# Kernel tuning notes

Hardware: AMD Instinct MI355X
Metric: run time of the kernel (lower is better)

The kernel has to match this reference:

```python
import jax, jax.numpy as jnp
import numpy as np

D_EMB = 512
N_HEADS = 8
D_K = 64
D_V = 64
D_FF = 2048
N_LAYERS = 6
VOCAB = 32000
SRC_LEN = 512


def sin_enc_table(n_position, d):
    pos = jnp.arange(n_position, dtype=jnp.float32)[:, None]
    j = jnp.arange(d, dtype=jnp.float32)[None, :]
    angle = pos / jnp.power(10000.0, 2.0 * jnp.floor(j / 2.0) / d)
    return jnp.where((jnp.arange(d) % 2 == 0)[None, :], jnp.sin(angle), jnp.cos(angle))


def layer_norm(x, gamma, beta, eps=1e-5):
    mu = jnp.mean(x, axis=-1, keepdims=True)
    var = jnp.mean(jnp.square(x - mu), axis=-1, keepdims=True)
    return (x - mu) * jax.lax.rsqrt(var + eps) * gamma + beta


def setup_inputs() -> dict:
    key = jax.random.key(0)
    ks = jax.random.split(key, 20)
    s = 0.02
    L = N_LAYERS
    inp = {
        'enc_inputs': jax.random.randint(ks[0], (16, 512), 0, VOCAB),
        'emb': jax.random.normal(ks[1], (VOCAB, D_EMB), jnp.float32) * s,
        'Wq': jax.random.normal(ks[2], (L, N_HEADS * D_K, D_EMB), jnp.float32) * s,
        'bq': jnp.zeros((L, N_HEADS * D_K), jnp.float32),
        'Wk': jax.random.normal(ks[3], (L, N_HEADS * D_K, D_EMB), jnp.float32) * s,
        'bk': jnp.zeros((L, N_HEADS * D_K), jnp.float32),
        'Wv': jax.random.normal(ks[4], (L, N_HEADS * D_V, D_EMB), jnp.float32) * s,
        'bv': jnp.zeros((L, N_HEADS * D_V), jnp.float32),
        'Wo': jax.random.normal(ks[5], (L, D_EMB, N_HEADS * D_V), jnp.float32) * s,
        'bo': jnp.zeros((L, D_EMB), jnp.float32),
        'g1': jnp.ones((L, D_EMB), jnp.float32),
        'b1': jnp.zeros((L, D_EMB), jnp.float32),
        'Wc1': jax.random.normal(ks[6], (L, D_FF, D_EMB), jnp.float32) * s,
        'bc1': jnp.zeros((L, D_FF), jnp.float32),
        'Wc2': jax.random.normal(ks[7], (L, D_EMB, D_FF), jnp.float32) * s,
        'bc2': jnp.zeros((L, D_EMB), jnp.float32),
        'g2': jnp.ones((L, D_EMB), jnp.float32),
        'b2': jnp.zeros((L, D_EMB), jnp.float32),
    }
    return inp


def encoder_fwd(enc_inputs, emb, Wq, bq, Wk, bk, Wv, bv, Wo, bo, g1, b1, Wc1, bc1, Wc2, bc2, g2, b2):
    B, S = enc_inputs.shape
    pos_table = sin_enc_table(SRC_LEN + 1, D_EMB)  # frozen
    x = emb[enc_inputs] + pos_table[jnp.arange(1, S + 1)][None, :, :]
    # pad mask: True where key token == 0; broadcast over heads and queries
    pad = (enc_inputs == 0)[:, None, None, :]  # [B,1,1,S]
    scale = 1.0 / np.sqrt(D_K)
    attn_weights = []
    for l in range(N_LAYERS):
        residual = x
        q = (x @ Wq[l].T + bq[l]).reshape(B, S, N_HEADS, D_K).transpose(0, 2, 1, 3)
        k = (x @ Wk[l].T + bk[l]).reshape(B, S, N_HEADS, D_K).transpose(0, 2, 1, 3)
        v = (x @ Wv[l].T + bv[l]).reshape(B, S, N_HEADS, D_V).transpose(0, 2, 1, 3)
        scores = jnp.einsum('bhqd,bhkd->bhqk', q, k) * scale
        scores = jnp.where(pad, -1e9, scores)
        w = jax.nn.softmax(scores, axis=-1)
        ctx = jnp.einsum('bhqk,bhkd->bhqd', w, v)
        ctx = ctx.transpose(0, 2, 1, 3).reshape(B, S, N_HEADS * D_V)
        x = layer_norm(ctx @ Wo[l].T + bo[l] + residual, g1[l], b1[l])
        # position-wise FFN (conv1d k=1 == dense)
        h = jax.nn.relu(x @ Wc1[l].T + bc1[l])
        x = layer_norm(h @ Wc2[l].T + bc2[l] + x, g2[l], b2[l])
        attn_weights.append(w)
    return x, jnp.stack(attn_weights)


def reference(enc_inputs, emb, Wq, bq, Wk, bk, Wv, bv, Wo, bo, g1, b1, Wc1, bc1, Wc2, bc2, g2, b2):
    return encoder_fwd(enc_inputs, emb, Wq, bq, Wk, bk, Wv, bv, Wo, bo, g1, b1, Wc1, bc1, Wc2, bc2, g2, b2)
```

## Files before the change

### kernel.cpp

```cpp
#include <hip/hip_runtime.h>

typedef unsigned short u16;
typedef __attribute__((ext_vector_type(8))) short s16x8;
typedef __attribute__((ext_vector_type(4))) float f32x4;
typedef __attribute__((ext_vector_type(4))) unsigned short u16x4;

#define DEVI __device__ __forceinline__

DEVI float bf2f(u16 h) { union { unsigned u; float f; } v; v.u = ((unsigned)h) << 16; return v.f; }
DEVI u16 f2bf(float f) {
  union { unsigned u; float f; } v; v.f = f;
  unsigned u = v.u;
  unsigned r = (u + 0x7fffu + ((u >> 16) & 1u)) >> 16;
  return (u16)r;
}

DEVI f32x4 mfma16(s16x8 a, s16x8 b, f32x4 c) {
  return __builtin_amdgcn_mfma_f32_16x16x32_bf16(a, b, c, 0, 0, 0);
}

__global__ void cvt_kern(const float* __restrict__ in, u16* __restrict__ out, int n4) {
  for (int i = blockIdx.x * blockDim.x + threadIdx.x; i < n4; i += gridDim.x * blockDim.x) {
    f32x4 v = ((const f32x4*)in)[i];
    u16x4 o = { f2bf(v[0]), f2bf(v[1]), f2bf(v[2]), f2bf(v[3]) };
    ((u16x4*)out)[i] = o;
  }
}

__global__ void cvt_qkv_kern(const float* __restrict__ Wq, const float* __restrict__ Wk,
                             const float* __restrict__ Wv, u16* __restrict__ Wout) {
  int total = 6 * 1536 * 512 / 8;
  for (int idx = blockIdx.x * blockDim.x + threadIdx.x; idx < total; idx += gridDim.x * blockDim.x) {
    int c8 = idx & 63;
    int t = idx >> 6;
    int r = t % 1536, l = t / 1536;
    const float* src; int rr = r;
    if (r < 512) src = Wq;
    else if (r < 1024) { src = Wk; rr = r - 512; }
    else { src = Wv; rr = r - 1024; }
    const f32x4* p = (const f32x4*)(src + ((size_t)(l * 512 + rr) * 512) + c8 * 8);
    f32x4 a = p[0], b = p[1];
    u16x4 o0 = { f2bf(a[0]), f2bf(a[1]), f2bf(a[2]), f2bf(a[3]) };
    u16x4 o1 = { f2bf(b[0]), f2bf(b[1]), f2bf(b[2]), f2bf(b[3]) };
    u16x4* q = (u16x4*)(Wout + (size_t)idx * 8);
    q[0] = o0; q[1] = o1;
  }
}

__global__ void biasqkv_kern(const float* __restrict__ bq, const float* __restrict__ bk,
                             const float* __restrict__ bv, float* __restrict__ bout) {
  int i = blockIdx.x * 256 + threadIdx.x;
  if (i >= 6 * 1536) return;
  int l = i / 1536, r = i % 1536;
  float v = (r < 512) ? bq[l * 512 + r] : (r < 1024) ? bk[l * 512 + r - 512] : bv[l * 512 + r - 1024];
  bout[i] = v;
}

__global__ void embed_kern(const int* __restrict__ tok, const float* __restrict__ emb,
                           float* __restrict__ x, u16* __restrict__ xb) {
  int bs = blockIdx.x;
  int s = bs & 511;
  int t = threadIdx.x;
  int id = tok[bs];
  float pos = (float)(s + 1);
  int j0 = t * 4;
  f32x4 e = *(const f32x4*)(emb + (size_t)id * 512 + j0);
  f32x4 o; u16x4 ob;
  #pragma unroll
  for (int u = 0; u < 4; ++u) {
    int j = j0 + u;
    float expo = (float)(j & ~1) * (1.0f / 512.0f);
    float ang = pos / powf(10000.0f, expo);
    float pe = (j & 1) ? cosf(ang) : sinf(ang);
    float v = e[u] + pe;
    o[u] = v; ob[u] = f2bf(v);
  }
  *(f32x4*)(x + (size_t)bs * 512 + j0) = o;
  *(u16x4*)(xb + (size_t)bs * 512 + j0) = ob;
}

template <int WM, bool RELU, bool F32OUT>
__global__ __launch_bounds__(256, 2) void gemm_bs(const u16* __restrict__ A,
                                                  const u16* __restrict__ Bt,
                                                  const float* __restrict__ bias,
                                                  float* __restrict__ Pf, u16* __restrict__ Cb,
                                                  int N, int K, int nN) {
  constexpr int MF = WM / 16;
  constexpr int RPB = WM * 4;
  __shared__ __align__(16) u16 Bsw[128 * 256];

  const int chunkw = gridDim.x >> 3;
  const int wgid = (blockIdx.x & 7) * chunkw + (blockIdx.x >> 3);
  const int n = wgid % nN, m = wgid / nN;
  const int bn0 = n * 128, bm0 = m * RPB;

  const int tid = threadIdx.x, lane = tid & 63, wid = tid >> 6;
  const int l15 = lane & 15, lhi = lane >> 4;
  const int mrow0 = bm0 + wid * WM;

  f32x4 acc[MF][8];
  #pragma unroll
  for (int i = 0; i < MF; ++i)
    #pragma unroll
    for (int j = 0; j < 8; ++j)
      #pragma unroll
      for (int r = 0; r < 4; ++r) acc[i][j][r] = 0.0f;

  const u16* aB[MF];
  #pragma unroll
  for (int i = 0; i < MF; ++i)
    aB[i] = A + (size_t)(mrow0 + i * 16 + l15) * K + lhi * 8;

  const int rounds = K >> 8;
  for (int r = 0; r < rounds; ++r) {
    const int kb = r << 8;
    s16x8 tmp[16];
    #pragma unroll
    for (int c = 0; c < 16; ++c) {
      int cc = c * 256 + tid;
      int row = cc >> 5, col = cc & 31;
      tmp[c] = *(const s16x8*)(Bt + (size_t)(bn0 + row) * K + kb + col * 8);
    }
    __syncthreads();
    #pragma unroll
    for (int c = 0; c < 16; ++c) {
      int cc = c * 256 + tid;
      int row = cc >> 5, col = cc & 31;
      int byte = row * 512 + ((col * 16) ^ ((row & 7) << 4));
      *(s16x8*)((char*)Bsw + byte) = tmp[c];
    }
    __syncthreads();
    #pragma unroll
    for (int ks = 0; ks < 8; ++ks) {
      s16x8 af[MF], bf[8];
      #pragma unroll
      for (int i = 0; i < MF; ++i)
        af[i] = *(const s16x8*)(aB[i] + kb + ks * 32);
      #pragma unroll
      for (int j = 0; j < 8; ++j) {
        int row = j * 16 + l15;
        int byte = row * 512 + (((ks * 64) + lhi * 16) ^ ((row & 7) << 4));
        bf[j] = *(const s16x8*)((char*)Bsw + byte);
      }
      #pragma unroll
      for (int i = 0; i < MF; ++i)
        #pragma unroll
        for (int j = 0; j < 8; ++j)
          acc[i][j] = mfma16(af[i], bf[j], acc[i][j]);
    }
  }

  const int r0 = mrow0 + lhi * 4;
  const int c0 = bn0 + l15;
  #pragma unroll
  for (int i = 0; i < MF; ++i)
    #pragma unroll
    for (int j = 0; j < 8; ++j) {
      int col = c0 + j * 16;
      float bv = F32OUT ? 0.0f : bias[col];
      #pragma unroll
      for (int r = 0; r < 4; ++r) {
        int row = r0 + i * 16 + r;
        float v = acc[i][j][r] + bv;
        if (RELU) v = fmaxf(v, 0.0f);
        if (F32OUT) Pf[(size_t)row * N + col] = v;
        else Cb[(size_t)row * N + col] = f2bf(v);
      }
    }
}

__global__ void ln2_kern(const float* __restrict__ parts,
                         const float* __restrict__ bias, const float* __restrict__ resid,
                         const float* __restrict__ gam, const float* __restrict__ bet,
                         float* __restrict__ out, u16* __restrict__ outb) {
  int row = blockIdx.x * 4 + (threadIdx.x >> 6);
  int t = threadIdx.x & 63;
  size_t base = (size_t)row * 512;
  const f32x4* p0 = (const f32x4*)(parts + base);
  f32x4 v0 = p0[t], v1 = p0[t + 64];
  const f32x4* bp2 = (const f32x4*)bias;
  f32x4 bia = bp2[t], bib = bp2[t + 64];
  const f32x4* rp = (const f32x4*)(resid + base);
  f32x4 rr0 = rp[t], rr1 = rp[t + 64];
  #pragma unroll
  for (int u = 0; u < 4; ++u) { v0[u] += bia[u] + rr0[u]; v1[u] += bib[u] + rr1[u]; }

  float s = v0[0] + v0[1] + v0[2] + v0[3] + v1[0] + v1[1] + v1[2] + v1[3];
  float q = v0[0]*v0[0] + v0[1]*v0[1] + v0[2]*v0[2] + v0[3]*v0[3]
          + v1[0]*v1[0] + v1[1]*v1[1] + v1[2]*v1[2] + v1[3]*v1[3];
  #pragma unroll
  for (int d = 1; d < 64; d <<= 1) { s += __shfl_xor(s, d, 64); q += __shfl_xor(q, d, 64); }
  float mu = s * (1.0f / 512.0f);
  float var = q * (1.0f / 512.0f) - mu * mu;
  float rs = rsqrtf(var + 1e-5f);
  const f32x4* gp = (const f32x4*)gam;
  const f32x4* bp = (const f32x4*)bet;
  f32x4 ga = gp[t], gb = gp[t + 64], ba = bp[t], bb = bp[t + 64];
  f32x4 o0, o1; u16x4 ob0, ob1;
  #pragma unroll
  for (int u = 0; u < 4; ++u) {
    float a0 = (v0[u] - mu) * rs * ga[u] + ba[u];
    float a1 = (v1[u] - mu) * rs * gb[u] + bb[u];
    o0[u] = a0; o1[u] = a1; ob0[u] = f2bf(a0); ob1[u] = f2bf(a1);
  }
  f32x4* op = (f32x4*)(out + base);
  op[t] = o0; op[t + 64] = o1;
  u16x4* obp = (u16x4*)(outb + base);
  obp[t] = ob0; obp[t + 64] = ob1;
}

__global__ void vtrans_kern(const u16* __restrict__ QKV, u16* __restrict__ Vt) {
  int bx = blockIdx.x;
  int st = bx & 7, h = (bx >> 3) & 7, b = bx >> 6;
  int s0 = st * 64;
  __shared__ __align__(16) u16 tile[64][72];
  int t = threadIdx.x;
  for (int c = t; c < 512; c += 256) {
    int r = c >> 3, cc = (c & 7) << 3;
    *(s16x8*)&tile[r][cc] =
        *(const s16x8*)&QKV[(size_t)(b * 512 + s0 + r) * 1536 + 1024 + h * 64 + cc];
  }
  __syncthreads();
  for (int c = t; c < 512; c += 256) {
    int d = c >> 3, sc = (c & 7) << 3;
    s16x8 o;
    #pragma unroll
    for (int i2 = 0; i2 < 8; ++i2) o[i2] = (short)tile[sc + i2][d];
    *(s16x8*)&Vt[((size_t)(b * 8 + h) * 64 + d) * 512 + s0 + sc] = o;
  }
}

__global__ void attn_kern(const u16* __restrict__ QKV, const u16* __restrict__ Vt,
                          const int* __restrict__ tok,
                          float* __restrict__ wout, u16* __restrict__ ctxb) {
  int bx = blockIdx.x;
  int qt = bx & 15;
  int h = (bx >> 4) & 7;
  int b = bx >> 7;
  int tid = threadIdx.x;
  int lane = tid & 63, wid = tid >> 6;
  int l15 = lane & 15, lhi = lane >> 4;
  int m0 = qt * 32;

  __shared__ __align__(16) u16 Wl[32][520];
  __shared__ float pmask[512];
  __shared__ float redbuf[2][32][4];

  for (int c = tid; c < 512; c += 256)
    pmask[c] = (tok[b * 512 + c] == 0) ? 1.0f : 0.0f;

  s16x8 qf[2][2];
  const u16* qbase = QKV + (size_t)(b * 512 + m0) * 1536 + h * 64;
  #pragma unroll
  for (int i = 0; i < 2; ++i)
    #pragma unroll
    for (int kk = 0; kk < 2; ++kk)
      qf[i][kk] = *(const s16x8*)(qbase + (size_t)(i * 16 + l15) * 1536 + kk * 32 + lhi * 8);

  f32x4 sacc[2][8];
  #pragma unroll
  for (int i = 0; i < 2; ++i)
    #pragma unroll
    for (int j = 0; j < 8; ++j)
      #pragma unroll
      for (int r = 0; r < 4; ++r) sacc[i][j][r] = 0.0f;

  int c0 = wid * 128;
  const u16* kbase = QKV + (size_t)(b * 512 + c0) * 1536 + 512 + h * 64;
  #pragma unroll
  for (int j = 0; j < 8; ++j) {
    #pragma unroll
    for (int kk = 0; kk < 2; ++kk) {
      s16x8 kf = *(const s16x8*)(kbase + (size_t)(j * 16 + l15) * 1536 + kk * 32 + lhi * 8);
      sacc[0][j] = mfma16(qf[0][kk], kf, sacc[0][j]);
      sacc[1][j] = mfma16(qf[1][kk], kf, sacc[1][j]);
    }
  }
  __syncthreads();

  float rm[2][4], sm[2][4], gi[2][4];
  #pragma unroll
  for (int i = 0; i < 2; ++i)
    #pragma unroll
    for (int r = 0; r < 4; ++r) rm[i][r] = -3.0e38f;

  #pragma unroll
  for (int j = 0; j < 8; ++j) {
    float pm = pmask[c0 + j * 16 + l15];
    #pragma unroll
    for (int i = 0; i < 2; ++i)
      #pragma unroll
      for (int r = 0; r < 4; ++r) {
        float sv = sacc[i][j][r] * 0.125f;
        sv = (pm != 0.0f) ? -1.0e9f : sv;
        sacc[i][j][r] = sv;
        rm[i][r] = fmaxf(rm[i][r], sv);
      }
  }
  #pragma unroll
  for (int d = 1; d < 16; d <<= 1)
    #pragma unroll
    for (int i = 0; i < 2; ++i)
      #pragma unroll
      for (int r = 0; r < 4; ++r)
        rm[i][r] = fmaxf(rm[i][r], __shfl_xor(rm[i][r], d, 64));

  if (l15 == 0) {
    #pragma unroll
    for (int i = 0; i < 2; ++i)
      #pragma unroll
      for (int r = 0; r < 4; ++r)
        redbuf[0][i * 16 + lhi * 4 + r][wid] = rm[i][r];
  }
  __syncthreads();
  #pragma unroll
  for (int i = 0; i < 2; ++i)
    #pragma unroll
    for (int r = 0; r < 4; ++r) {
      int row = i * 16 + lhi * 4 + r;
      rm[i][r] = fmaxf(fmaxf(redbuf[0][row][0], redbuf[0][row][1]),
                       fmaxf(redbuf[0][row][2], redbuf[0][row][3]));
      sm[i][r] = 0.0f;
    }
  #pragma unroll
  for (int j = 0; j < 8; ++j)
    #pragma unroll
    for (int i = 0; i < 2; ++i)
      #pragma unroll
      for (int r = 0; r < 4; ++r) {
        float pv = __expf(sacc[i][j][r] - rm[i][r]);
        sacc[i][j][r] = pv;
        sm[i][r] += pv;
      }
  #pragma unroll
  for (int d = 1; d < 16; d <<= 1)
    #pragma unroll
    for (int i = 0; i < 2; ++i)
      #pragma unroll
      for (int r = 0; r < 4; ++r)
        sm[i][r] += __shfl_xor(sm[i][r], d, 64);
  if (l15 == 0) {
    #pragma unroll
    for (int i = 0; i < 2; ++i)
      #pragma unroll
      for (int r = 0; r < 4; ++r)
        redbuf[1][i * 16 + lhi * 4 + r][wid] = sm[i][r];
  }
  __syncthreads();
  #pragma unroll
  for (int i = 0; i < 2; ++i)
    #pragma unroll
    for (int r = 0; r < 4; ++r) {
      int row = i * 16 + lhi * 4 + r;
      float tot = redbuf[1][row][0] + redbuf[1][row][1] + redbuf[1][row][2] + redbuf[1][row][3];
      gi[i][r] = 1.0f / tot;
    }

  #pragma unroll
  for (int j = 0; j < 8; ++j)
    #pragma unroll
    for (int i = 0; i < 2; ++i)
      #pragma unroll
      for (int r = 0; r < 4; ++r)
        Wl[i * 16 + lhi * 4 + r][c0 + j * 16 + l15] = f2bf(sacc[i][j][r] * gi[i][r]);
  __syncthreads();

  float* wrow = wout + ((size_t)((b * 8 + h) * 512 + m0)) * 512;
  for (int c = tid; c < 2048; c += 256) {
    int rr = c >> 6;
    int cc = (c & 63) << 3;
    s16x8 wv = *(const s16x8*)&Wl[rr][cc];
    f32x4 f0 = { bf2f((u16)wv[0]), bf2f((u16)wv[1]), bf2f((u16)wv[2]), bf2f((u16)wv[3]) };
    f32x4 f1 = { bf2f((u16)wv[4]), bf2f((u16)wv[5]), bf2f((u16)wv[6]), bf2f((u16)wv[7]) };
    *(f32x4*)(wrow + (size_t)rr * 512 + cc) = f0;
    *(f32x4*)(wrow + (size_t)rr * 512 + cc + 4) = f1;
  }

  f32x4 cacc[2];
  #pragma unroll
  for (int i = 0; i < 2; ++i)
    #pragma unroll
    for (int r = 0; r < 4; ++r) cacc[i][r] = 0.0f;
  const u16* vbase = Vt + ((size_t)((b * 8 + h) * 64 + wid * 16 + l15)) * 512;
  #pragma unroll
  for (int kk = 0; kk < 16; ++kk) {
    s16x8 vf = *(const s16x8*)(vbase + kk * 32 + lhi * 8);
    #pragma unroll
    for (int i = 0; i < 2; ++i) {
      s16x8 wf = *(const s16x8*)&Wl[i * 16 + l15][kk * 32 + lhi * 8];
      cacc[i] = mfma16(wf, vf, cacc[i]);
    }
  }
  #pragma unroll
  for (int i = 0; i < 2; ++i)
    #pragma unroll
    for (int r = 0; r < 4; ++r)
      ctxb[(size_t)(b * 512 + m0 + i * 16 + lhi * 4 + r) * 512 + h * 64 + wid * 16 + l15] =
          f2bf(cacc[i][r]);
}

extern "C" void kernel_launch(void* const* d_in, const int* in_sizes, int n_in,
                              void* d_out, int out_size, void* d_ws, size_t ws_size,
                              hipStream_t stream) {
  const int*   tok = (const int*)d_in[0];
  const float* emb = (const float*)d_in[1];
  const float* Wq  = (const float*)d_in[2];
  const float* bq  = (const float*)d_in[3];
  const float* Wk  = (const float*)d_in[4];
  const float* bk  = (const float*)d_in[5];
  const float* Wv  = (const float*)d_in[6];
  const float* bv  = (const float*)d_in[7];
  const float* Wo  = (const float*)d_in[8];
  const float* bo  = (const float*)d_in[9];
  const float* g1  = (const float*)d_in[10];
  const float* b1  = (const float*)d_in[11];
  const float* Wc1 = (const float*)d_in[12];
  const float* bc1 = (const float*)d_in[13];
  const float* Wc2 = (const float*)d_in[14];
  const float* bc2 = (const float*)d_in[15];
  const float* g2  = (const float*)d_in[16];
  const float* b2  = (const float*)d_in[17];
  (void)in_sizes; (void)n_in; (void)out_size; (void)ws_size;

  float* out_x = (float*)d_out;
  float* out_w = out_x + (size_t)16 * 512 * 512;

  char* p = (char*)d_ws;
  size_t off = 0;
  auto alloc = [&](size_t bytes) { char* r = p + off; off += (bytes + 255) & ~(size_t)255; return r; };
  u16*   xb  = (u16*)alloc((size_t)8192 * 512 * 2);
  float* xf  = (float*)alloc((size_t)8192 * 512 * 4);
  float* parts = (float*)alloc((size_t)8192 * 512 * 4);
  char*  regA = alloc((size_t)8192 * 1536 * 2 + (size_t)8192 * 512 * 2);
  u16* QKVb = (u16*)regA;
  u16* Vtb  = QKVb + (size_t)8192 * 1536;
  u16* hb   = (u16*)regA;
  u16* ctxb = (u16*)alloc((size_t)8192 * 512 * 2);
  u16* Wqkvb = (u16*)alloc((size_t)6 * 1536 * 512 * 2);
  u16* Wob   = (u16*)alloc((size_t)6 * 512 * 512 * 2);
  u16* Wc1b  = (u16*)alloc((size_t)6 * 2048 * 512 * 2);
  u16* Wc2b  = (u16*)alloc((size_t)6 * 2048 * 512 * 2);
  float* bqkvb = (float*)alloc((size_t)6 * 1536 * 4);

  cvt_qkv_kern<<<1024, 256, 0, stream>>>(Wq, Wk, Wv, Wqkvb);
  biasqkv_kern<<<36, 256, 0, stream>>>(bq, bk, bv, bqkvb);
  cvt_kern<<<1024, 256, 0, stream>>>(Wo,  Wob,  6 * 512 * 512 / 4);
  cvt_kern<<<1024, 256, 0, stream>>>(Wc1, Wc1b, 6 * 2048 * 512 / 4);
  cvt_kern<<<1024, 256, 0, stream>>>(Wc2, Wc2b, 6 * 2048 * 512 / 4);

  embed_kern<<<8192, 128, 0, stream>>>(tok, emb, xf, xb);

  for (int l = 0; l < 6; ++l) {
    const u16* wqkv_l = Wqkvb + (size_t)l * 1536 * 512;
    const u16* wo_l = Wob + (size_t)l * 512 * 512;
    const u16* w1_l = Wc1b + (size_t)l * 2048 * 512;
    const u16* w2_l = Wc2b + (size_t)l * 2048 * 512;

    gemm_bs<32, false, false><<<768, 256, 0, stream>>>(xb, wqkv_l, bqkvb + l * 1536,
                                                       nullptr, QKVb, 1536, 512, 12);
    vtrans_kern<<<1024, 256, 0, stream>>>(QKVb, Vtb);
    attn_kern<<<2048, 256, 0, stream>>>(QKVb, Vtb, tok,
                                        out_w + (size_t)l * 8 * 16 * 512 * 512, ctxb);
    gemm_bs<16, false, true><<<512, 256, 0, stream>>>(ctxb, wo_l, nullptr,
                                                      parts, nullptr, 512, 512, 4);
    ln2_kern<<<2048, 256, 0, stream>>>(parts, bo + l * 512, xf,
                                       g1 + l * 512, b1 + l * 512, xf, xb);
    gemm_bs<32, true, false><<<1024, 256, 0, stream>>>(xb, w1_l, bc1 + l * 2048,
                                                       nullptr, hb, 2048, 512, 16);
    gemm_bs<16, false, true><<<512, 256, 0, stream>>>(hb, w2_l, nullptr,
                                                      parts, nullptr, 512, 2048, 4);
    ln2_kern<<<2048, 256, 0, stream>>>(parts, bc2 + l * 512, xf,
                                       g2 + l * 512, b2 + l * 512, (l == 5 ? out_x : xf), xb);
  }
}
```

Baseline: 1.178 ms.

## Fuse V transpose into QKV GEMM epilogue and LayerNorm into output GEMMs

The QKV GEMM now writes the V section straight into the transposed Vt layout from its epilogue, which removes the separate vtrans kernel. A new gemmln kernel computes a full 16x512 row tile per block, then adds bias and residual and applies LayerNorm in place. This removes the fp32 partials buffer and the standalone ln2 passes after the Wo and Wc2 GEMMs. The fused kernel uses a narrow M tile, reloads the whole B matrix per block without double buffering, and issues strided scalar stores, which may lower GEMM efficiency. The in-place residual read and output write on xf are row-local, so they stay safe.

```diff
diff --git a/kernel.cpp b/kernel.cpp
--- a/kernel.cpp
+++ b/kernel.cpp
@@ -79,11 +79,11 @@
   *(u16x4*)(xb + (size_t)bs * 512 + j0) = ob;
 }
 
-template <int WM, bool RELU, bool F32OUT>
+template <int WM, bool RELU, bool VTOUT>
 __global__ __launch_bounds__(256, 2) void gemm_bs(const u16* __restrict__ A,
                                                   const u16* __restrict__ Bt,
                                                   const float* __restrict__ bias,
-                                                  float* __restrict__ Pf, u16* __restrict__ Cb,
+                                                  u16* __restrict__ Cb, u16* __restrict__ Vt,
                                                   int N, int K, int nN) {
   constexpr int MF = WM / 16;
   constexpr int RPB = WM * 4;
@@ -152,81 +152,140 @@
 
   const int r0 = mrow0 + lhi * 4;
   const int c0 = bn0 + l15;
-  #pragma unroll
-  for (int i = 0; i < MF; ++i)
-    #pragma unroll
-    for (int j = 0; j < 8; ++j) {
-      int col = c0 + j * 16;
-      float bv = F32OUT ? 0.0f : bias[col];
-      #pragma unroll
-      for (int r = 0; r < 4; ++r) {
-        int row = r0 + i * 16 + r;
-        float v = acc[i][j][r] + bv;
-        if (RELU) v = fmaxf(v, 0.0f);
-        if (F32OUT) Pf[(size_t)row * N + col] = v;
-        else Cb[(size_t)row * N + col] = f2bf(v);
+  if (VTOUT && bn0 >= 1024) {
+    #pragma unroll
+    for (int i = 0; i < MF; ++i)
+      #pragma unroll
+      for (int j = 0; j < 8; ++j) {
+        int col = c0 + j * 16;
+        float bv = bias[col];
+        int hc = col - 1024;
+        int grow = r0 + i * 16;
+        int b = grow >> 9, s = grow & 511;
+        u16x4 pk;
+        #pragma unroll
+        for (int r = 0; r < 4; ++r) pk[r] = f2bf(acc[i][j][r] + bv);
+        *(u16x4*)&Vt[((size_t)((b * 8 + (hc >> 6)) * 64 + (hc & 63))) * 512 + s] = pk;
       }
-    }
-}
-
-__global__ void ln2_kern(const float* __restrict__ parts,
-                         const float* __restrict__ bias, const float* __restrict__ resid,
-                         const float* __restrict__ gam, const float* __restrict__ bet,
-                         float* __restrict__ out, u16* __restrict__ outb) {
-  int row = blockIdx.x * 4 + (threadIdx.x >> 6);
-  int t = threadIdx.x & 63;
-  size_t base = (size_t)row * 512;
-  const f32x4* p0 = (const f32x4*)(parts + base);
-  f32x4 v0 = p0[t], v1 = p0[t + 64];
-  const f32x4* bp2 = (const f32x4*)bias;
-  f32x4 bia = bp2[t], bib = bp2[t + 64];
-  const f32x4* rp = (const f32x4*)(resid + base);
-  f32x4 rr0 = rp[t], rr1 = rp[t + 64];
-  #pragma unroll
-  for (int u = 0; u < 4; ++u) { v0[u] += bia[u] + rr0[u]; v1[u] += bib[u] + rr1[u]; }
-
-  float s = v0[0] + v0[1] + v0[2] + v0[3] + v1[0] + v1[1] + v1[2] + v1[3];
-  float q = v0[0]*v0[0] + v0[1]*v0[1] + v0[2]*v0[2] + v0[3]*v0[3]
-          + v1[0]*v1[0] + v1[1]*v1[1] + v1[2]*v1[2] + v1[3]*v1[3];
-  #pragma unroll
-  for (int d = 1; d < 64; d <<= 1) { s += __shfl_xor(s, d, 64); q += __shfl_xor(q, d, 64); }
-  float mu = s * (1.0f / 512.0f);
-  float var = q * (1.0f / 512.0f) - mu * mu;
-  float rs = rsqrtf(var + 1e-5f);
-  const f32x4* gp = (const f32x4*)gam;
-  const f32x4* bp = (const f32x4*)bet;
-  f32x4 ga = gp[t], gb = gp[t + 64], ba = bp[t], bb = bp[t + 64];
-  f32x4 o0, o1; u16x4 ob0, ob1;
-  #pragma unroll
-  for (int u = 0; u < 4; ++u) {
-    float a0 = (v0[u] - mu) * rs * ga[u] + ba[u];
-    float a1 = (v1[u] - mu) * rs * gb[u] + bb[u];
-    o0[u] = a0; o1[u] = a1; ob0[u] = f2bf(a0); ob1[u] = f2bf(a1);
-  }
-  f32x4* op = (f32x4*)(out + base);
-  op[t] = o0; op[t + 64] = o1;
-  u16x4* obp = (u16x4*)(outb + base);
-  obp[t] = ob0; obp[t + 64] = ob1;
-}
-
-__global__ void vtrans_kern(const u16* __restrict__ QKV, u16* __restrict__ Vt) {
-  int bx = blockIdx.x;
-  int st = bx & 7, h = (bx >> 3) & 7, b = bx >> 6;
-  int s0 = st * 64;
-  __shared__ __align__(16) u16 tile[64][72];
-  int t = threadIdx.x;
-  for (int c = t; c < 512; c += 256) {
-    int r = c >> 3, cc = (c & 7) << 3;
-    *(s16x8*)&tile[r][cc] =
-        *(const s16x8*)&QKV[(size_t)(b * 512 + s0 + r) * 1536 + 1024 + h * 64 + cc];
+  } else {
+    #pragma unroll
+    for (int i = 0; i < MF; ++i)
+      #pragma unroll
+      for (int j = 0; j < 8; ++j) {
+        int col = c0 + j * 16;
+        float bv = bias[col];
+        #pragma unroll
+        for (int r = 0; r < 4; ++r) {
+          int row = r0 + i * 16 + r;
+          float v = acc[i][j][r] + bv;
+          if (RELU) v = fmaxf(v, 0.0f);
+          Cb[(size_t)row * N + col] = f2bf(v);
+        }
+      }
+  }
+}
+
+__global__ __launch_bounds__(256, 2) void gemmln_kern(
+    const u16* __restrict__ A, const u16* __restrict__ Bt,
+    const float* __restrict__ bias, const float* __restrict__ resid,
+    const float* __restrict__ gam, const float* __restrict__ bet,
+    float* __restrict__ outf, u16* __restrict__ outb, int K) {
+  __shared__ __align__(16) u16 Bsw[512 * 64];
+  __shared__ float red[16][4][2];
+  const int row0 = blockIdx.x * 16;
+  const int tid = threadIdx.x, lane = tid & 63, wid = tid >> 6;
+  const int l15 = lane & 15, lhi = lane >> 4;
+  const int c0 = wid * 128;
+
+  f32x4 acc[8];
+  #pragma unroll
+  for (int j = 0; j < 8; ++j)
+    #pragma unroll
+    for (int r = 0; r < 4; ++r) acc[j][r] = 0.0f;
+
+  const u16* aP = A + (size_t)(row0 + l15) * K + lhi * 8;
+
+  const int rounds = K >> 6;
+  for (int r = 0; r < rounds; ++r) {
+    const int kb = r << 6;
+    s16x8 tmp[16];
+    #pragma unroll
+    for (int c = 0; c < 16; ++c) {
+      int cc = c * 256 + tid;
+      int row = cc >> 3, ch = cc & 7;
+      tmp[c] = *(const s16x8*)(Bt + (size_t)row * K + kb + ch * 8);
+    }
+    __syncthreads();
+    #pragma unroll
+    for (int c = 0; c < 16; ++c) {
+      int cc = c * 256 + tid;
+      int row = cc >> 3, ch = cc & 7;
+      int byte = row * 128 + ((ch * 16) ^ ((row & 7) << 4));
+      *(s16x8*)((char*)Bsw + byte) = tmp[c];
+    }
+    __syncthreads();
+    #pragma unroll
+    for (int ks = 0; ks < 2; ++ks) {
+      s16x8 af = *(const s16x8*)(aP + kb + ks * 32);
+      #pragma unroll
+      for (int j = 0; j < 8; ++j) {
+        int row = c0 + j * 16 + l15;
+        int byte = row * 128 + (((ks * 64) + lhi * 16) ^ ((row & 7) << 4));
+        s16x8 bf = *(const s16x8*)((char*)Bsw + byte);
+        acc[j] = mfma16(af, bf, acc[j]);
+      }
+    }
+  }
+
+  float s[4] = {0, 0, 0, 0}, q[4] = {0, 0, 0, 0};
+  #pragma unroll
+  for (int j = 0; j < 8; ++j) {
+    int col = c0 + j * 16 + l15;
+    float bv = bias[col];
+    #pragma unroll
+    for (int r = 0; r < 4; ++r) {
+      int row = row0 + lhi * 4 + r;
+      float v = acc[j][r] + bv + resid[(size_t)row * 512 + col];
+      acc[j][r] = v;
+      s[r] += v; q[r] += v * v;
+    }
+  }
+  #pragma unroll
+  for (int d = 1; d < 16; d <<= 1)
+    #pragma unroll
+    for (int r = 0; r < 4; ++r) {
+      s[r] += __shfl_xor(s[r], d, 64);
+      q[r] += __shfl_xor(q[r], d, 64);
+    }
+  if (l15 == 0) {
+    #pragma unroll
+    for (int r = 0; r < 4; ++r) {
+      red[lhi * 4 + r][wid][0] = s[r];
+      red[lhi * 4 + r][wid][1] = q[r];
+    }
   }
   __syncthreads();
-  for (int c = t; c < 512; c += 256) {
-    int d = c >> 3, sc = (c & 7) << 3;
-    s16x8 o;
-    #pragma unroll
-    for (int i2 = 0; i2 < 8; ++i2) o[i2] = (short)tile[sc + i2][d];
-    *(s16x8*)&Vt[((size_t)(b * 8 + h) * 64 + d) * 512 + s0 + sc] = o;
+  float mu[4], rs[4];
+  #pragma unroll
+  for (int r = 0; r < 4; ++r) {
+    int row = lhi * 4 + r;
+    float S = red[row][0][0] + red[row][1][0] + red[row][2][0] + red[row][3][0];
+    float Q = red[row][0][1] + red[row][1][1] + red[row][2][1] + red[row][3][1];
+    mu[r] = S * (1.0f / 512.0f);
+    float var = Q * (1.0f / 512.0f) - mu[r] * mu[r];
+    rs[r] = rsqrtf(var + 1e-5f);
+  }
+  #pragma unroll
+  for (int j = 0; j < 8; ++j) {
+    int col = c0 + j * 16 + l15;
+    float ga = gam[col], be = bet[col];
+    #pragma unroll
+    for (int r = 0; r < 4; ++r) {
+      int row = row0 + lhi * 4 + r;
+      float o = (acc[j][r] - mu[r]) * rs[r] * ga + be;
+      outf[(size_t)row * 512 + col] = o;
+      outb[(size_t)row * 512 + col] = f2bf(o);
+    }
   }
 }
 
@@ -430,7 +489,6 @@
   auto alloc = [&](size_t bytes) { char* r = p + off; off += (bytes + 255) & ~(size_t)255; return r; };
   u16*   xb  = (u16*)alloc((size_t)8192 * 512 * 2);
   float* xf  = (float*)alloc((size_t)8192 * 512 * 4);
-  float* parts = (float*)alloc((size_t)8192 * 512 * 4);
   char*  regA = alloc((size_t)8192 * 1536 * 2 + (size_t)8192 * 512 * 2);
   u16* QKVb = (u16*)regA;
   u16* Vtb  = QKVb + (size_t)8192 * 1536;
@@ -456,20 +514,16 @@
     const u16* w1_l = Wc1b + (size_t)l * 2048 * 512;
     const u16* w2_l = Wc2b + (size_t)l * 2048 * 512;
 
-    gemm_bs<32, false, false><<<768, 256, 0, stream>>>(xb, wqkv_l, bqkvb + l * 1536,
-                                                       nullptr, QKVb, 1536, 512, 12);
-    vtrans_kern<<<1024, 256, 0, stream>>>(QKVb, Vtb);
+    gemm_bs<32, false, true><<<768, 256, 0, stream>>>(xb, wqkv_l, bqkvb + l * 1536,
+                                                      QKVb, Vtb, 1536, 512, 12);
     attn_kern<<<2048, 256, 0, stream>>>(QKVb, Vtb, tok,
                                         out_w + (size_t)l * 8 * 16 * 512 * 512, ctxb);
-    gemm_bs<16, false, true><<<512, 256, 0, stream>>>(ctxb, wo_l, nullptr,
-                                                      parts, nullptr, 512, 512, 4);
-    ln2_kern<<<2048, 256, 0, stream>>>(parts, bo + l * 512, xf,
-                                       g1 + l * 512, b1 + l * 512, xf, xb);
+    gemmln_kern<<<512, 256, 0, stream>>>(ctxb, wo_l, bo + l * 512, xf,
+                                         g1 + l * 512, b1 + l * 512, xf, xb, 512);
     gemm_bs<32, true, false><<<1024, 256, 0, stream>>>(xb, w1_l, bc1 + l * 2048,
-                                                       nullptr, hb, 2048, 512, 16);
-    gemm_bs<16, false, true><<<512, 256, 0, stream>>>(hb, w2_l, nullptr,
-                                                      parts, nullptr, 512, 2048, 4);
-    ln2_kern<<<2048, 256, 0, stream>>>(parts, bc2 + l * 512, xf,
-                                       g2 + l * 512, b2 + l * 512, (l == 5 ? out_x : xf), xb);
-  }
-}
+                                                       hb, nullptr, 2048, 512, 16);
+    gemmln_kern<<<512, 256, 0, stream>>>(hb, w2_l, bc2 + l * 512, xf,
+                                         g2 + l * 512, b2 + l * 512,
+                                         (l == 5 ? out_x : xf), xb, 2048);
+  }
+}
```

Result: slower. 1.326 ms (+12.6%).
